# Kernel optimization log

Measured on AMD Instinct MI355X. Metric: run time of the kernel, lower is better.

The kernel has to match this reference:

```python
import jax, jax.numpy as jnp
import numpy as np

DIM = 512
DIM_INPUTS = (8,)*4 + (16,)*4 + (32,)*4 + (64,)*4 + (128,)*4 + (256,)*4  # 24 bands, sum=2016
N_BANDS = len(DIM_INPUTS)
TOTAL_OUT2 = 2 * sum(DIM_INPUTS)  # 4032 (concatenated last-layer gated width)
B, T = 4, 512


def _glu_tanh(z):
    # LinearGLUWithTanH epilogue: chunk last dim, tanh(a) * sigmoid(gate)
    a, gate = jnp.split(z, 2, axis=-1)
    return jnp.tanh(a) * jax.nn.sigmoid(gate)


def setup_inputs() -> dict:
    key = jax.random.key(0)
    k0, k1, k2, k3, k4 = jax.random.split(key, 5)
    x = jax.random.normal(k0, (B, T, N_BANDS, DIM), dtype=jnp.float32)
    # layer 0: per-band Linear(DIM, 2*DIM), stacked over bands
    W0 = jax.random.normal(k1, (N_BANDS, DIM, 2 * DIM), dtype=jnp.float32) / np.float32(np.sqrt(DIM))
    b0 = jax.random.normal(k2, (N_BANDS, 2 * DIM), dtype=jnp.float32) * 0.01
    # layer 1 (last): per-band Linear(DIM, 2*dim_in); widths differ, so pack
    # all bands' weight columns into one concatenated matrix sliced statically.
    W1 = jax.random.normal(k3, (DIM, TOTAL_OUT2), dtype=jnp.float32) / np.float32(np.sqrt(DIM))
    b1 = jax.random.normal(k4, (TOTAL_OUT2,), dtype=jnp.float32) * 0.01
    return {"x": x, "W0": W0, "b0": b0, "W1": W1, "b1": b1}


def reference(x, W0, b0, W1, b1):
    # layer 0 for all bands in one grouped GEMM: (b t n d),(n d e)->(b t n e)
    h = _glu_tanh(jnp.einsum('btnd,nde->btne', x, W0) + b0)  # (B,T,N,DIM)
    outs = []
    off = 0
    for i, di in enumerate(DIM_INPUTS):  # static loop over structurally distinct bands
        w = W1[:, off:off + 2 * di]
        bb = b1[off:off + 2 * di]
        outs.append(_glu_tanh(h[:, :, i] @ w + bb))  # (B,T,di)
        off += 2 * di
    return jnp.concatenate(outs, axis=-1)  # (B,T,sum(DIM_INPUTS))
```

## Files before the change

### kernel.cpp

```cpp
#include <hip/hip_runtime.h>
#include <cstdint>
#include <cstddef>


typedef _Float16 f16;
typedef _Float16 f16x8 __attribute__((ext_vector_type(8)));
typedef float floatx4 __attribute__((ext_vector_type(4)));

#define BT 2048
#define NB 24

__device__ __forceinline__ int band_di(int b){ return 8 << (b >> 2); }
__device__ __forceinline__ int band_off2(int b){
  int g = b >> 2;
  return 2 * (32 * ((1 << g) - 1) + (b & 3) * (8 << g));
}

__device__ __forceinline__ float fsigm(float x){
  return __builtin_amdgcn_rcpf(1.f + __expf(-x));
}
__device__ __forceinline__ float ftanh(float x){
  return 1.f - 2.f * __builtin_amdgcn_rcpf(1.f + __expf(2.f * x));
}

__device__ __forceinline__ void gl_lds16(const void* g, void* l){
  __builtin_amdgcn_global_load_lds(
      (const __attribute__((address_space(1))) unsigned int*)g,
      (__attribute__((address_space(3))) unsigned int*)l, 16, 0, 0);
}

__global__ __launch_bounds__(256) void prep(const float* __restrict__ x,
                                            const float* __restrict__ W0,
                                            const float* __restrict__ W1,
                                            const float* __restrict__ b0,
                                            const float* __restrict__ b1,
                                            f16* __restrict__ xh2,
                                            f16* __restrict__ w0t,
                                            f16* __restrict__ w1t,
                                            float* __restrict__ b0p,
                                            float* __restrict__ b1p){
  __shared__ __align__(16) char smem[33792];
  int bid = blockIdx.x;
  int t = threadIdx.x;
  if (bid < 6144){
    int r = bid / 3, bg = bid - 3 * r;
    int band = bg * 8 + (t >> 5);
    int k16 = (t & 31) * 16;
    const float* src = x + ((size_t)(r * 24 + band)) * 512 + k16;
    float4 v0 = *(const float4*)(src + 0);
    float4 v1 = *(const float4*)(src + 4);
    float4 v2 = *(const float4*)(src + 8);
    float4 v3 = *(const float4*)(src + 12);
    f16x8 o0 = { (f16)v0.x,(f16)v0.y,(f16)v0.z,(f16)v0.w,
                 (f16)v1.x,(f16)v1.y,(f16)v1.z,(f16)v1.w };
    f16x8 o1 = { (f16)v2.x,(f16)v2.y,(f16)v2.z,(f16)v2.w,
                 (f16)v3.x,(f16)v3.y,(f16)v3.z,(f16)v3.w };
    f16* dst = xh2 + ((size_t)(band * 2048 + r)) * 512 + k16;
    *(f16x8*)(dst + 0) = o0;
    *(f16x8*)(dst + 8) = o1;
  } else if (bid < 12288){
    float (*tile)[33] = (float(*)[33])smem;
    int b2 = bid - 6144;
    int dt   = b2 & 7;
    int half = (b2 >> 3) & 1;
    int g    = (b2 >> 4) & 15;
    int band = b2 >> 8;
    int c0 = half * 512 + g * 32;
    int d0 = dt * 64;
    int r  = t >> 2;
    int cs = (t & 3) * 8;
    const float* src = W0 + ((size_t)(band * 512 + d0 + r)) * 1024 + c0 + cs;
    float4 v0 = *(const float4*)src;
    float4 v1 = *(const float4*)(src + 4);
    tile[r][cs+0]=v0.x; tile[r][cs+1]=v0.y; tile[r][cs+2]=v0.z; tile[r][cs+3]=v0.w;
    tile[r][cs+4]=v1.x; tile[r][cs+5]=v1.y; tile[r][cs+6]=v1.z; tile[r][cs+7]=v1.w;
    __syncthreads();
    int i   = t >> 3;
    int ds8 = (t & 7) * 8;
    int prow = g * 64 + 2 * i + half;
    f16x8 o;
    #pragma unroll
    for (int k = 0; k < 8; ++k) o[k] = (f16)tile[ds8 + k][i];
    *(f16x8*)(w0t + ((size_t)(band * 1024 + prow)) * 512 + d0 + ds8) = o;
  } else if (bid < 12540){
    f16 (*tw)[520] = (f16(*)[520])smem;
    int jt = bid - 12288;
    int j16 = jt * 16;
    int band = 23;
    for (int b = 0; b < 24; ++b){ if (j16 < band_off2(b + 1)) { band = b; break; } }
    int off2 = band_off2(band), di = band_di(band);
    int p0 = j16 - off2;
    int oca = off2 + (p0 >> 1);
    int ocg = oca + di;
    #pragma unroll
    for (int hh = 0; hh < 2; ++hh){
      int d = hh * 256 + t;
      const float* rowp = W1 + (size_t)d * 4032;
      float4 a0 = *(const float4*)(rowp + oca);
      float4 a1 = *(const float4*)(rowp + oca + 4);
      float4 g0 = *(const float4*)(rowp + ocg);
      float4 g1 = *(const float4*)(rowp + ocg + 4);
      float av[8] = {a0.x,a0.y,a0.z,a0.w,a1.x,a1.y,a1.z,a1.w};
      float gv[8] = {g0.x,g0.y,g0.z,g0.w,g1.x,g1.y,g1.z,g1.w};
      #pragma unroll
      for (int q = 0; q < 8; ++q){
        tw[2*q][d]   = (f16)av[q];
        tw[2*q+1][d] = (f16)gv[q];
      }
    }
    __syncthreads();
    int j = t & 15, dc = (t >> 4) * 32;
    f16x8 o[4];
    #pragma unroll
    for (int k = 0; k < 4; ++k) o[k] = *(const f16x8*)&tw[j][dc + k*8];
    f16* dst = w1t + (size_t)(j16 + j) * 512 + dc;
    #pragma unroll
    for (int k = 0; k < 4; ++k) *(f16x8*)(dst + k*8) = o[k];
  } else {
    int idx = (bid - 12540) * 256 + t;
    if (idx < NB * 1024){
      int p = idx & 1023;
      int base = idx & ~1023;
      b0p[idx] = b0[base + ((p & 1) ? 512 + (p >> 1) : (p >> 1))];
    } else {
      int j = idx - NB * 1024;
      if (j < 4032){
        int band = 23;
        for (int b = 0; b < 24; ++b){ if (j < band_off2(b + 1)) { band = b; break; } }
        int off2 = band_off2(band);
        int di = band_di(band);
        int p = j - off2;
        b1p[j] = b1[off2 + ((p & 1) ? di + (p >> 1) : (p >> 1))];
      }
    }
  }
}

__global__ __launch_bounds__(256) void gemm1(const f16* __restrict__ xh2,
                                             const f16* __restrict__ w0t,
                                             const float* __restrict__ b0p,
                                             f16* __restrict__ h){
  __shared__ __align__(16) f16 As[128 * 64];
  __shared__ __align__(16) f16 Bs[128 * 64];
  int bid = blockIdx.x;
  int wid = (bid & 7) * 384 + (bid >> 3);
  int band = wid >> 7;
  int mt = (wid >> 3) & 15;
  int nt = wid & 7;
  int t = threadIdx.x;
  int lane = t & 63, w = t >> 6;
  int wm = w & 1, wn = w >> 1;
  int quad = lane >> 4, lc = lane & 15;
  const int mrow0 = mt * 128;
  const int nrow0 = nt * 128;

  const char* gA[4]; const char* gB[4];
  f16* lA[4]; f16* lB[4];
  #pragma unroll
  for (int p = 0; p < 4; ++p){
    int idx = p * 256 + t;
    int r = idx >> 3, s = idx & 7, l = s ^ (r & 7);
    gA[p] = (const char*)(xh2 + ((size_t)(band * 2048 + mrow0 + r)) * 512 + l * 8);
    gB[p] = (const char*)(w0t + ((size_t)(band * 1024 + nrow0 + r)) * 512 + l * 8);
    lA[p] = &As[idx * 8];
    lB[p] = &Bs[idx * 8];
  }
  int aoff[4], boff[4];
  #pragma unroll
  for (int i = 0; i < 4; ++i){
    int m = wm * 64 + i * 16 + lc;
    aoff[i] = (m * 64 + ((quad ^ (m & 7)) << 3)) * 2;
    int n = wn * 64 + i * 16 + lc;
    boff[i] = (n * 64 + ((quad ^ (n & 7)) << 3)) * 2;
  }
  const char* Ab = (const char*)As;
  const char* Bb = (const char*)Bs;

  floatx4 acc[4][4];
  #pragma unroll
  for (int i = 0; i < 4; ++i)
    #pragma unroll
    for (int j = 0; j < 4; ++j) acc[i][j] = floatx4{0.f, 0.f, 0.f, 0.f};

  for (int kb = 0; kb < 8; ++kb){
    #pragma unroll
    for (int p = 0; p < 4; ++p){ gl_lds16(gA[p], lA[p]); gA[p] += 128; }
    #pragma unroll
    for (int p = 0; p < 4; ++p){ gl_lds16(gB[p], lB[p]); gB[p] += 128; }
    __syncthreads();
    #pragma unroll
    for (int s2 = 0; s2 < 2; ++s2){
      f16x8 af[4], bf[4];
      #pragma unroll
      for (int i = 0; i < 4; ++i){
        af[i] = *(const f16x8*)(Ab + (aoff[i] ^ (s2 * 64)));
        bf[i] = *(const f16x8*)(Bb + (boff[i] ^ (s2 * 64)));
      }
      #pragma unroll
      for (int i = 0; i < 4; ++i)
        #pragma unroll
        for (int j = 0; j < 4; ++j)
          acc[i][j] = __builtin_amdgcn_mfma_f32_16x16x32_f16(af[i], bf[j], acc[i][j], 0, 0, 0);
    }
    __syncthreads();
  }
  #pragma unroll
  for (int j = 0; j < 4; ++j){
    int colp = nrow0 + wn * 64 + j * 16 + lc;
    float bias = b0p[band * 1024 + colp];
    #pragma unroll
    for (int i = 0; i < 4; ++i){
      int mbase = mrow0 + wm * 64 + i * 16 + quad * 4;
      #pragma unroll
      for (int r = 0; r < 4; ++r){
        float z = acc[i][j][r] + bias;
        float v = (lc & 1) ? fsigm(z) : ftanh(z);
        float vp = __shfl_xor(v, 1);
        if (!(lc & 1)){
          h[((size_t)band * BT + mbase + r) * 512 + (colp >> 1)] = (f16)(v * vp);
        }
      }
    }
  }
}

template<int BN>
__device__ __forceinline__ void gemm2_tile(const f16* __restrict__ hb,
                                           const f16* __restrict__ w1t,
                                           const float* __restrict__ b1p,
                                           float* __restrict__ out,
                                           int band, int mt, int ntile,
                                           f16* As, f16* Bs){
  constexpr int WNW = (BN == 128) ? 2 : 1;
  constexpr int WMW = 4 / WNW;
  constexpr int MF = 128 / (WMW * 16);
  constexpr int NF = BN / (WNW * 16);
  int t = threadIdx.x;
  int lane = t & 63, w = t >> 6;
  int wm = (WNW == 2) ? (w & 1) : w;
  int wn = (WNW == 2) ? (w >> 1) : 0;
  int quad = lane >> 4, lc = lane & 15;
  int off2 = band_off2(band);
  int jbase = off2 + ntile * BN;

  constexpr int BCH = BN * 8;
  constexpr int BP = (BCH + 255) / 256;
  const char* gA[4]; const char* gB[BP];
  f16* lA[4]; f16* lB[BP];
  #pragma unroll
  for (int p = 0; p < 4; ++p){
    int idx = p * 256 + t;
    int r = idx >> 3, s = idx & 7, l = s ^ (r & 7);
    gA[p] = (const char*)(hb + ((size_t)(mt * 128 + r)) * 512 + l * 8);
    lA[p] = &As[idx * 8];
  }
  #pragma unroll
  for (int p = 0; p < BP; ++p){
    int idx = p * 256 + t;
    int r = idx >> 3, s = idx & 7, l = s ^ (r & 7);
    gB[p] = (const char*)(w1t + ((size_t)(jbase + r)) * 512 + l * 8);
    lB[p] = &Bs[idx * 8];
  }
  int aoff[MF], boff[NF];
  #pragma unroll
  for (int i = 0; i < MF; ++i){
    int m = wm * (MF * 16) + i * 16 + lc;
    aoff[i] = (m * 64 + ((quad ^ (m & 7)) << 3)) * 2;
  }
  #pragma unroll
  for (int j = 0; j < NF; ++j){
    int n = wn * (NF * 16) + j * 16 + lc;
    boff[j] = (n * 64 + ((quad ^ (n & 7)) << 3)) * 2;
  }
  const char* Ab = (const char*)As;
  const char* Bb = (const char*)Bs;

  floatx4 acc[MF][NF];
  #pragma unroll
  for (int i = 0; i < MF; ++i)
    #pragma unroll
    for (int j = 0; j < NF; ++j) acc[i][j] = floatx4{0.f, 0.f, 0.f, 0.f};

  for (int kb = 0; kb < 8; ++kb){
    #pragma unroll
    for (int p = 0; p < 4; ++p){ gl_lds16(gA[p], lA[p]); gA[p] += 128; }
    #pragma unroll
    for (int p = 0; p < BP; ++p){
      if ((BCH % 256 == 0) || (p * 256 + t) < BCH){
        gl_lds16(gB[p], lB[p]); gB[p] += 128;
      }
    }
    __syncthreads();
    #pragma unroll
    for (int s2 = 0; s2 < 2; ++s2){
      f16x8 af[MF], bf[NF];
      #pragma unroll
      for (int i = 0; i < MF; ++i)
        af[i] = *(const f16x8*)(Ab + (aoff[i] ^ (s2 * 64)));
      #pragma unroll
      for (int j = 0; j < NF; ++j)
        bf[j] = *(const f16x8*)(Bb + (boff[j] ^ (s2 * 64)));
      #pragma unroll
      for (int i = 0; i < MF; ++i)
        #pragma unroll
        for (int j = 0; j < NF; ++j)
          acc[i][j] = __builtin_amdgcn_mfma_f32_16x16x32_f16(af[i], bf[j], acc[i][j], 0, 0, 0);
    }
    __syncthreads();
  }
  int outbase = off2 >> 1;
  #pragma unroll
  for (int j = 0; j < NF; ++j){
    int p = ntile * BN + wn * (NF * 16) + j * 16 + lc;
    float bias = b1p[off2 + p];
    #pragma unroll
    for (int i = 0; i < MF; ++i){
      int mbase = mt * 128 + wm * (MF * 16) + i * 16 + quad * 4;
      #pragma unroll
      for (int r = 0; r < 4; ++r){
        float z = acc[i][j][r] + bias;
        float v = (lc & 1) ? fsigm(z) : ftanh(z);
        float vp = __shfl_xor(v, 1);
        if (!(lc & 1)){
          out[(size_t)(mbase + r) * 2016 + outbase + (p >> 1)] = v * vp;
        }
      }
    }
  }
}

__global__ __launch_bounds__(256) void gemm2(const f16* __restrict__ h,
                                             const f16* __restrict__ w1t,
                                             const float* __restrict__ b1p,
                                             float* __restrict__ out){
  __shared__ __align__(16) f16 As[128 * 64];
  __shared__ __align__(16) f16 Bs[128 * 64];
  int bid0 = blockIdx.x;
  int bid = (bid0 & 7) * 80 + (bid0 >> 3);
  int band, mt, ntile, cls;
  if (bid < 256){
    band = bid >> 4; mt = bid & 15; ntile = 0; cls = band >> 2;
  } else if (bid < 384){
    int rel = bid - 256; band = 16 + (rel >> 5);
    int r2 = rel & 31; mt = r2 & 15; ntile = r2 >> 4; cls = 4;
  } else {
    int rel = bid - 384; band = 20 + (rel >> 6);
    int r2 = rel & 63; mt = r2 & 15; ntile = r2 >> 4; cls = 5;
  }
  const f16* hb = h + ((size_t)band << 20);
  switch (cls){
    case 0:  gemm2_tile<16 >(hb, w1t, b1p, out, band, mt, ntile, As, Bs); break;
    case 1:  gemm2_tile<32 >(hb, w1t, b1p, out, band, mt, ntile, As, Bs); break;
    case 2:  gemm2_tile<64 >(hb, w1t, b1p, out, band, mt, ntile, As, Bs); break;
    default: gemm2_tile<128>(hb, w1t, b1p, out, band, mt, ntile, As, Bs); break;
  }
}

extern "C" void kernel_launch(void* const* d_in, const int* in_sizes, int n_in,
                              void* d_out, int out_size, void* d_ws, size_t ws_size,
                              hipStream_t stream){
  const float* x  = (const float*)d_in[0];
  const float* W0 = (const float*)d_in[1];
  const float* b0 = (const float*)d_in[2];
  const float* W1 = (const float*)d_in[3];
  const float* b1 = (const float*)d_in[4];
  char* ws = (char*)d_ws;
  f16*   xh2  = (f16*)(ws);
  f16*   hbuf = (f16*)(ws + 50331648);
  f16*   w0t  = (f16*)(ws + 100663296);
  f16*   w1t  = (f16*)(ws + 125829120);
  float* b0p  = (float*)(ws + 129957888);
  float* b1p  = (float*)(ws + 130056192);

  prep <<<12652, 256, 0, stream>>>(x, W0, W1, b0, b1, xh2, w0t, w1t, b0p, b1p);
  gemm1<<<3072,  256, 0, stream>>>(xh2, w0t, b0p, hbuf);
  gemm2<<<640,   256, 0, stream>>>(hbuf, w1t, b1p, (float*)d_out);
}
```

Before: 333.3 us.

## Split prep into plain x cast and weight prep; shrink gemm2 M tile

The x conversion no longer transposes to band-major layout. It becomes a simple contiguous fp16 cast, and gemm1 reads A rows with a stride of 24 bands instead. The weight and bias prep moves to a separate kernel. gemm2 now uses 64-row M tiles with 1280 blocks instead of 128-row tiles with 640, to raise parallelism for the narrow bands. The trade-offs are less contiguous A loads in gemm1, one extra kernel launch, and less reuse of the B tile in gemm2.

```diff
diff --git a/kernel.cpp b/kernel.cpp
--- a/kernel.cpp
+++ b/kernel.cpp
@@ -29,42 +29,33 @@
       (__attribute__((address_space(3))) unsigned int*)l, 16, 0, 0);
 }
 
-__global__ __launch_bounds__(256) void prep(const float* __restrict__ x,
-                                            const float* __restrict__ W0,
-                                            const float* __restrict__ W1,
-                                            const float* __restrict__ b0,
-                                            const float* __restrict__ b1,
-                                            f16* __restrict__ xh2,
-                                            f16* __restrict__ w0t,
-                                            f16* __restrict__ w1t,
-                                            float* __restrict__ b0p,
-                                            float* __restrict__ b1p){
-  __shared__ __align__(16) char smem[33792];
+__global__ __launch_bounds__(256) void cast_x(const float4* __restrict__ in,
+                                              f16* __restrict__ out){
+  int t = blockIdx.x * 256 + threadIdx.x;
+  float4 v0 = in[2 * t];
+  float4 v1 = in[2 * t + 1];
+  f16x8 o = { (f16)v0.x,(f16)v0.y,(f16)v0.z,(f16)v0.w,
+              (f16)v1.x,(f16)v1.y,(f16)v1.z,(f16)v1.w };
+  *(f16x8*)(out + (size_t)t * 8) = o;
+}
+
+__global__ __launch_bounds__(256) void cast_w(const float* __restrict__ W0,
+                                              const float* __restrict__ W1,
+                                              const float* __restrict__ b0,
+                                              const float* __restrict__ b1,
+                                              f16* __restrict__ w0t,
+                                              f16* __restrict__ w1t,
+                                              float* __restrict__ b0p,
+                                              float* __restrict__ b1p){
+  __shared__ __align__(16) char smem[16640];
   int bid = blockIdx.x;
   int t = threadIdx.x;
   if (bid < 6144){
-    int r = bid / 3, bg = bid - 3 * r;
-    int band = bg * 8 + (t >> 5);
-    int k16 = (t & 31) * 16;
-    const float* src = x + ((size_t)(r * 24 + band)) * 512 + k16;
-    float4 v0 = *(const float4*)(src + 0);
-    float4 v1 = *(const float4*)(src + 4);
-    float4 v2 = *(const float4*)(src + 8);
-    float4 v3 = *(const float4*)(src + 12);
-    f16x8 o0 = { (f16)v0.x,(f16)v0.y,(f16)v0.z,(f16)v0.w,
-                 (f16)v1.x,(f16)v1.y,(f16)v1.z,(f16)v1.w };
-    f16x8 o1 = { (f16)v2.x,(f16)v2.y,(f16)v2.z,(f16)v2.w,
-                 (f16)v3.x,(f16)v3.y,(f16)v3.z,(f16)v3.w };
-    f16* dst = xh2 + ((size_t)(band * 2048 + r)) * 512 + k16;
-    *(f16x8*)(dst + 0) = o0;
-    *(f16x8*)(dst + 8) = o1;
-  } else if (bid < 12288){
     float (*tile)[33] = (float(*)[33])smem;
-    int b2 = bid - 6144;
-    int dt   = b2 & 7;
-    int half = (b2 >> 3) & 1;
-    int g    = (b2 >> 4) & 15;
-    int band = b2 >> 8;
+    int dt   = bid & 7;
+    int half = (bid >> 3) & 1;
+    int g    = (bid >> 4) & 15;
+    int band = bid >> 8;
     int c0 = half * 512 + g * 32;
     int d0 = dt * 64;
     int r  = t >> 2;
@@ -82,9 +73,9 @@
     #pragma unroll
     for (int k = 0; k < 8; ++k) o[k] = (f16)tile[ds8 + k][i];
     *(f16x8*)(w0t + ((size_t)(band * 1024 + prow)) * 512 + d0 + ds8) = o;
-  } else if (bid < 12540){
+  } else if (bid < 6396){
     f16 (*tw)[520] = (f16(*)[520])smem;
-    int jt = bid - 12288;
+    int jt = bid - 6144;
     int j16 = jt * 16;
     int band = 23;
     for (int b = 0; b < 24; ++b){ if (j16 < band_off2(b + 1)) { band = b; break; } }
@@ -117,7 +108,7 @@
     #pragma unroll
     for (int k = 0; k < 4; ++k) *(f16x8*)(dst + k*8) = o[k];
   } else {
-    int idx = (bid - 12540) * 256 + t;
+    int idx = (bid - 6396) * 256 + t;
     if (idx < NB * 1024){
       int p = idx & 1023;
       int base = idx & ~1023;
@@ -136,7 +127,7 @@
   }
 }
 
-__global__ __launch_bounds__(256) void gemm1(const f16* __restrict__ xh2,
+__global__ __launch_bounds__(256) void gemm1(const f16* __restrict__ xh,
                                              const f16* __restrict__ w0t,
                                              const float* __restrict__ b0p,
                                              f16* __restrict__ h){
@@ -160,7 +151,7 @@
   for (int p = 0; p < 4; ++p){
     int idx = p * 256 + t;
     int r = idx >> 3, s = idx & 7, l = s ^ (r & 7);
-    gA[p] = (const char*)(xh2 + ((size_t)(band * 2048 + mrow0 + r)) * 512 + l * 8);
+    gA[p] = (const char*)(xh + ((size_t)(mrow0 + r) * 24 + band) * 512 + l * 8);
     gB[p] = (const char*)(w0t + ((size_t)(band * 1024 + nrow0 + r)) * 512 + l * 8);
     lA[p] = &As[idx * 8];
     lB[p] = &Bs[idx * 8];
@@ -231,27 +222,25 @@
                                            float* __restrict__ out,
                                            int band, int mt, int ntile,
                                            f16* As, f16* Bs){
-  constexpr int WNW = (BN == 128) ? 2 : 1;
-  constexpr int WMW = 4 / WNW;
-  constexpr int MF = 128 / (WMW * 16);
-  constexpr int NF = BN / (WNW * 16);
+  constexpr int MF = (BN == 128) ? 2 : 1;
+  constexpr int NF = (BN == 128) ? 4 : BN / 16;
   int t = threadIdx.x;
   int lane = t & 63, w = t >> 6;
-  int wm = (WNW == 2) ? (w & 1) : w;
-  int wn = (WNW == 2) ? (w >> 1) : 0;
+  int wrow = (BN == 128) ? (w & 1) : w;
+  int wcol = (BN == 128) ? (w >> 1) : 0;
   int quad = lane >> 4, lc = lane & 15;
   int off2 = band_off2(band);
   int jbase = off2 + ntile * BN;
 
-  constexpr int BCH = BN * 8;
-  constexpr int BP = (BCH + 255) / 256;
-  const char* gA[4]; const char* gB[BP];
-  f16* lA[4]; f16* lB[BP];
-  #pragma unroll
-  for (int p = 0; p < 4; ++p){
+  constexpr int BU = BN * 8;
+  constexpr int BP = (BU + 255) / 256;
+  const char* gA[2]; const char* gB[BP];
+  f16* lA[2]; f16* lB[BP];
+  #pragma unroll
+  for (int p = 0; p < 2; ++p){
     int idx = p * 256 + t;
     int r = idx >> 3, s = idx & 7, l = s ^ (r & 7);
-    gA[p] = (const char*)(hb + ((size_t)(mt * 128 + r)) * 512 + l * 8);
+    gA[p] = (const char*)(hb + ((size_t)(mt * 64 + r)) * 512 + l * 8);
     lA[p] = &As[idx * 8];
   }
   #pragma unroll
@@ -264,12 +253,12 @@
   int aoff[MF], boff[NF];
   #pragma unroll
   for (int i = 0; i < MF; ++i){
-    int m = wm * (MF * 16) + i * 16 + lc;
+    int m = wrow * (MF * 16) + i * 16 + lc;
     aoff[i] = (m * 64 + ((quad ^ (m & 7)) << 3)) * 2;
   }
   #pragma unroll
   for (int j = 0; j < NF; ++j){
-    int n = wn * (NF * 16) + j * 16 + lc;
+    int n = wcol * 64 + j * 16 + lc;
     boff[j] = (n * 64 + ((quad ^ (n & 7)) << 3)) * 2;
   }
   const char* Ab = (const char*)As;
@@ -283,10 +272,10 @@
 
   for (int kb = 0; kb < 8; ++kb){
     #pragma unroll
-    for (int p = 0; p < 4; ++p){ gl_lds16(gA[p], lA[p]); gA[p] += 128; }
+    for (int p = 0; p < 2; ++p){ gl_lds16(gA[p], lA[p]); gA[p] += 128; }
     #pragma unroll
     for (int p = 0; p < BP; ++p){
-      if ((BCH % 256 == 0) || (p * 256 + t) < BCH){
+      if ((BU % 256 == 0) || (p * 256 + t) < BU){
         gl_lds16(gB[p], lB[p]); gB[p] += 128;
       }
     }
@@ -311,11 +300,11 @@
   int outbase = off2 >> 1;
   #pragma unroll
   for (int j = 0; j < NF; ++j){
-    int p = ntile * BN + wn * (NF * 16) + j * 16 + lc;
+    int p = ntile * BN + wcol * 64 + j * 16 + lc;
     float bias = b1p[off2 + p];
     #pragma unroll
     for (int i = 0; i < MF; ++i){
-      int mbase = mt * 128 + wm * (MF * 16) + i * 16 + quad * 4;
+      int mbase = mt * 64 + wrow * (MF * 16) + i * 16 + quad * 4;
       #pragma unroll
       for (int r = 0; r < 4; ++r){
         float z = acc[i][j][r] + bias;
@@ -333,22 +322,21 @@
                                              const f16* __restrict__ w1t,
                                              const float* __restrict__ b1p,
                                              float* __restrict__ out){
-  __shared__ __align__(16) f16 As[128 * 64];
+  __shared__ __align__(16) f16 As[64 * 64];
   __shared__ __align__(16) f16 Bs[128 * 64];
-  int bid0 = blockIdx.x;
-  int bid = (bid0 & 7) * 80 + (bid0 >> 3);
-  int band, mt, ntile, cls;
-  if (bid < 256){
-    band = bid >> 4; mt = bid & 15; ntile = 0; cls = band >> 2;
-  } else if (bid < 384){
-    int rel = bid - 256; band = 16 + (rel >> 5);
-    int r2 = rel & 31; mt = r2 & 15; ntile = r2 >> 4; cls = 4;
+  int bid = blockIdx.x;
+  int band, mt, ntile, g;
+  if (bid < 512){
+    g = bid >> 7; band = g * 4 + ((bid >> 5) & 3); mt = bid & 31; ntile = 0;
+  } else if (bid < 768){
+    int rel = bid - 512; band = 16 + (rel >> 6);
+    mt = rel & 31; ntile = (rel >> 5) & 1; g = 3;
   } else {
-    int rel = bid - 384; band = 20 + (rel >> 6);
-    int r2 = rel & 63; mt = r2 & 15; ntile = r2 >> 4; cls = 5;
+    int rel = bid - 768; band = 20 + (rel >> 7);
+    mt = rel & 31; ntile = (rel >> 5) & 3; g = 3;
   }
   const f16* hb = h + ((size_t)band << 20);
-  switch (cls){
+  switch (g){
     case 0:  gemm2_tile<16 >(hb, w1t, b1p, out, band, mt, ntile, As, Bs); break;
     case 1:  gemm2_tile<32 >(hb, w1t, b1p, out, band, mt, ntile, As, Bs); break;
     case 2:  gemm2_tile<64 >(hb, w1t, b1p, out, band, mt, ntile, As, Bs); break;
@@ -365,14 +353,15 @@
   const float* W1 = (const float*)d_in[3];
   const float* b1 = (const float*)d_in[4];
   char* ws = (char*)d_ws;
-  f16*   xh2  = (f16*)(ws);
+  f16*   xh   = (f16*)(ws);
   f16*   hbuf = (f16*)(ws + 50331648);
   f16*   w0t  = (f16*)(ws + 100663296);
   f16*   w1t  = (f16*)(ws + 125829120);
   float* b0p  = (float*)(ws + 129957888);
   float* b1p  = (float*)(ws + 130056192);
 
-  prep <<<12652, 256, 0, stream>>>(x, W0, W1, b0, b1, xh2, w0t, w1t, b0p, b1p);
-  gemm1<<<3072,  256, 0, stream>>>(xh2, w0t, b0p, hbuf);
-  gemm2<<<640,   256, 0, stream>>>(hbuf, w1t, b1p, (float*)d_out);
-}
+  cast_x<<<12288, 256, 0, stream>>>((const float4*)x, xh);
+  cast_w<<<6508,  256, 0, stream>>>(W0, W1, b0, b1, w0t, w1t, b0p, b1p);
+  gemm1 <<<3072,  256, 0, stream>>>(xh, w0t, b0p, hbuf);
+  gemm2 <<<1280,  256, 0, stream>>>(hbuf, w1t, b1p, (float*)d_out);
+}
```

Measured after the change: 329.4 us. Within noise of the previous version (-1.2%).
